# Performance work log

Measured on AMD Instinct MI355X. Metric: run time of the kernel, lower is better.

## Reference

```python
import jax, jax.numpy as jnp
import numpy as np

B, K, T, C = 4, 8, 2048, 64

def setup_inputs() -> dict:
    key = jax.random.key(0)
    ks = jax.random.split(key, 7)
    return {
        "x": jax.random.normal(ks[0], (B, K, T, C), dtype=jnp.float32),
        "Wq": jax.random.normal(ks[1], (C, C), dtype=jnp.float32) / np.sqrt(C),
        "bq": jax.random.normal(ks[2], (C,), dtype=jnp.float32) * 0.01,
        "Wk": jax.random.normal(ks[3], (C, C), dtype=jnp.float32) / np.sqrt(C),
        "bk": jax.random.normal(ks[4], (C,), dtype=jnp.float32) * 0.01,
        "Wv": jax.random.normal(ks[5], (C, C), dtype=jnp.float32) / np.sqrt(C),
        "bv": jax.random.normal(ks[6], (C,), dtype=jnp.float32) * 0.01,
    }

def reference(x, Wq, bq, Wk, bk, Wv, bv):
    c_dim = x.shape[-1]
    # torch nn.Linear: y = x @ W.T + b
    q = jnp.einsum('bktc,dc->bktd', x, Wq) + bq
    k = jnp.einsum('bktc,dc->bktd', x, Wk) + bk
    v = jnp.einsum('bktc,dc->bktd', x, Wv) + bv
    scores = jnp.einsum('bkic,bkjc->bkij', q, k) / jnp.sqrt(jnp.float32(c_dim))
    attn = jax.nn.softmax(scores, axis=-1)
    out = jnp.einsum('bkij,bkjc->bkic', attn, v)
    return out
```

## Files before the change

### kernel.cpp

```cpp
#include <hip/hip_runtime.h>


#define T_DIM 2048
#define NHEAD 32
#define NKT   (T_DIM / 64)
#define QSCALE 0.18033688011112042f
#define SOFF  8.0f

#define SWZ(row, grp) ((row) * 64 + ((((grp) ^ ((row) & 7)) & 7) * 8) + (((grp) & 8) * 8))

typedef _Float16 h8 __attribute__((ext_vector_type(8)));
typedef _Float16 h4 __attribute__((ext_vector_type(4)));
typedef __fp16   g2 __attribute__((ext_vector_type(2)));
typedef float    f4 __attribute__((ext_vector_type(4)));

union H4U { h4 v; g2 p[2]; };

__device__ inline h4 cvt4(f4 x) {
    H4U u;
    u.p[0] = __builtin_amdgcn_cvt_pkrtz(x[0], x[1]);
    u.p[1] = __builtin_amdgcn_cvt_pkrtz(x[2], x[3]);
    return u.v;
}

__global__ __launch_bounds__(256) void qkv_proj_kernel(
    const float* __restrict__ x,
    const float* __restrict__ Wq, const float* __restrict__ bq,
    const float* __restrict__ Wk, const float* __restrict__ bk,
    const float* __restrict__ Wv, const float* __restrict__ bv,
    _Float16* __restrict__ qh, _Float16* __restrict__ kh,
    _Float16* __restrict__ vt)
{
    __shared__ _Float16 xs[128 * 64];
    __shared__ _Float16 ws[3][64 * 64];
    __shared__ _Float16 ot[128 * 64];
    __shared__ float bsh[3][64];

    const int tid  = threadIdx.x;
    const int row0 = blockIdx.x * 128;
    const int head = blockIdx.x >> 4;
    const int t0   = (blockIdx.x & 15) * 128;

    {
        const float* xb = x + (size_t)row0 * 64;
        #pragma unroll
        for (int pass = 0; pass < 8; ++pass) {
            const int idx = pass * 1024 + tid * 4;
            const int r = idx >> 6, c = idx & 63;
            f4 xv = *(const f4*)(xb + idx);
            *(h4*)&xs[SWZ(r, c >> 3) + (c & 7)] = cvt4(xv);
        }
    }
    #pragma unroll
    for (int m = 0; m < 3; ++m) {
        const float* Wm = (m == 0) ? Wq : ((m == 1) ? Wk : Wv);
        const float* bm = (m == 0) ? bq : ((m == 1) ? bk : bv);
        #pragma unroll
        for (int pass = 0; pass < 4; ++pass) {
            const int idx = pass * 1024 + tid * 4;
            const int d = idx >> 6, c = idx & 63;
            f4 wv = *(const f4*)(Wm + idx);
            *(h4*)&ws[m][SWZ(d, c >> 3) + (c & 7)] = cvt4(wv);
        }
        if (tid < 64) bsh[m][tid] = bm[tid];
    }
    __syncthreads();

    const int w    = tid >> 6;
    const int lane = tid & 63;
    const int l15  = lane & 15;
    const int qd   = lane >> 4;

    h8 af[2][2];
    #pragma unroll
    for (int mt = 0; mt < 2; ++mt)
        #pragma unroll
        for (int ch = 0; ch < 2; ++ch) {
            const int r = w * 32 + mt * 16 + l15;
            af[mt][ch] = *(const h8*)&xs[SWZ(r, ch * 4 + qd)];
        }

    #pragma unroll
    for (int m = 0; m < 3; ++m) {
        h8 bf[4][2];
        #pragma unroll
        for (int ns = 0; ns < 4; ++ns)
            #pragma unroll
            for (int ch = 0; ch < 2; ++ch)
                bf[ns][ch] = *(const h8*)&ws[m][SWZ(ns * 16 + l15, ch * 4 + qd)];

        f4 acc[2][4];
        #pragma unroll
        for (int mt = 0; mt < 2; ++mt)
            #pragma unroll
            for (int ns = 0; ns < 4; ++ns)
                acc[mt][ns] = (f4){0.f, 0.f, 0.f, 0.f};
        #pragma unroll
        for (int ch = 0; ch < 2; ++ch)
            #pragma unroll
            for (int mt = 0; mt < 2; ++mt)
                #pragma unroll
                for (int ns = 0; ns < 4; ++ns)
                    acc[mt][ns] = __builtin_amdgcn_mfma_f32_16x16x32_f16(
                        af[mt][ch], bf[ns][ch], acc[mt][ns], 0, 0, 0);

        __syncthreads();
        if (m < 2) {
            #pragma unroll
            for (int mt = 0; mt < 2; ++mt)
                #pragma unroll
                for (int ns = 0; ns < 4; ++ns) {
                    const int d = ns * 16 + l15;
                    const float bias = bsh[m][d];
                    #pragma unroll
                    for (int r = 0; r < 4; ++r) {
                        const int t = w * 32 + mt * 16 + qd * 4 + r;
                        float v = acc[mt][ns][r] + bias;
                        if (m == 0) v *= QSCALE;
                        ot[SWZ(t, d >> 3) + (d & 7)] = (_Float16)v;
                    }
                }
            __syncthreads();
            _Float16* dst = (m == 0) ? qh : kh;
            #pragma unroll
            for (int pass = 0; pass < 4; ++pass) {
                const int t  = pass * 32 + (tid >> 3);
                const int c0 = (tid & 7) * 8;
                *(h8*)&dst[(size_t)(row0 + t) * 64 + c0] =
                    *(const h8*)&ot[SWZ(t, tid & 7)];
            }
        } else {
            #pragma unroll
            for (int mt = 0; mt < 2; ++mt)
                #pragma unroll
                for (int ns = 0; ns < 4; ++ns) {
                    const int d = ns * 16 + l15;
                    const float bias = bsh[2][d];
                    const int tl = w * 32 + mt * 16 + qd * 4;
                    h4 pv;
                    #pragma unroll
                    for (int r = 0; r < 4; ++r)
                        pv[r] = (_Float16)(acc[mt][ns][r] + bias);
                    const int g = tl >> 3;
                    *(h4*)&ot[d * 128 + ((g ^ (d & 7)) & 7) * 8 + ((g & 8) * 8) + (tl & 7)] = pv;
                }
            __syncthreads();
            #pragma unroll
            for (int pass = 0; pass < 4; ++pass) {
                const int idx = pass * 2048 + tid * 8;
                const int d = idx >> 7, tl = idx & 127;
                const int g = tl >> 3;
                h8 val = *(const h8*)&ot[d * 128 + ((g ^ (d & 7)) & 7) * 8 + ((g & 8) * 8)];
                *(h8*)&vt[(size_t)(head * 64 + d) * T_DIM + t0 + tl] = val;
            }
        }
    }
}

__global__ __launch_bounds__(256) void attn_kernel(
    const _Float16* __restrict__ qh, const _Float16* __restrict__ kh,
    const _Float16* __restrict__ vt, float* __restrict__ out)
{
    __shared__ _Float16 kts[64 * 64];
    __shared__ _Float16 vts[64 * 64];
    const int tid  = threadIdx.x;
    const int w    = tid >> 6;
    const int lane = tid & 63;
    const int l15  = lane & 15;
    const int qd   = lane >> 4;
    const int head = blockIdx.x >> 4;
    const int qt   = blockIdx.x & 15;
    const int q0   = qt * 128 + w * 32;

    h8 qf[2][2];
    #pragma unroll
    for (int is = 0; is < 2; ++is) {
        const _Float16* qp = qh + (size_t)(head * T_DIM + q0 + is * 16 + l15) * 64 + qd * 8;
        qf[is][0] = *(const h8*)qp;
        qf[is][1] = *(const h8*)(qp + 32);
    }

    float l_s[2] = {0.f, 0.f};
    f4 oacc[2][4];
    #pragma unroll
    for (int is = 0; is < 2; ++is)
        #pragma unroll
        for (int cs = 0; cs < 4; ++cs)
            oacc[is][cs] = (f4){0.f, 0.f, 0.f, 0.f};

    const size_t kbase = (size_t)head * T_DIM * 64;
    const int srow = tid >> 3;
    const int sgrp = tid & 7;
    const _Float16* kg = kh + kbase + (size_t)srow * 64 + sgrp * 8;
    const _Float16* vg = vt + kbase + (size_t)srow * T_DIM + sgrp * 8;
    _Float16* kl0 = &kts[SWZ(srow, sgrp)];
    _Float16* kl1 = &kts[SWZ(srow + 32, sgrp)];
    _Float16* vl0 = &vts[SWZ(srow, sgrp)];
    _Float16* vl1 = &vts[SWZ(srow + 32, sgrp)];

    h8 kr0 = *(const h8*)(kg);
    h8 kr1 = *(const h8*)(kg + (size_t)32 * 64);
    h8 vr0 = *(const h8*)(vg);
    h8 vr1 = *(const h8*)(vg + (size_t)32 * T_DIM);

    for (int kt = 0; kt < NKT; ++kt) {
        __syncthreads();
        *(h8*)kl0 = kr0; *(h8*)kl1 = kr1;
        *(h8*)vl0 = vr0; *(h8*)vl1 = vr1;
        __syncthreads();
        if (kt + 1 < NKT) {
            const _Float16* kg1 = kg + (size_t)(kt + 1) * 4096;
            const _Float16* vg1 = vg + (size_t)(kt + 1) * 64;
            kr0 = *(const h8*)(kg1);
            kr1 = *(const h8*)(kg1 + (size_t)32 * 64);
            vr0 = *(const h8*)(vg1);
            vr1 = *(const h8*)(vg1 + (size_t)32 * T_DIM);
        }

        f4 st[4][2];
        #pragma unroll
        for (int jt = 0; jt < 4; ++jt)
            #pragma unroll
            for (int is = 0; is < 2; ++is)
                st[jt][is] = (f4){-SOFF, -SOFF, -SOFF, -SOFF};
        #pragma unroll
        for (int ch = 0; ch < 2; ++ch)
            #pragma unroll
            for (int jt = 0; jt < 4; ++jt) {
                h8 kf = *(const h8*)&kts[SWZ(jt * 16 + l15, ch * 4 + qd)];
                #pragma unroll
                for (int is = 0; is < 2; ++is)
                    st[jt][is] = __builtin_amdgcn_mfma_f32_16x16x32_f16(
                        kf, qf[is][ch], st[jt][is], 0, 0, 0);
            }

        h4 pf[4][2];
        #pragma unroll
        for (int is = 0; is < 2; ++is) {
            float rs = 0.f;
            #pragma unroll
            for (int jt = 0; jt < 4; ++jt) {
                float p0 = __builtin_exp2f(st[jt][is][0]);
                float p1 = __builtin_exp2f(st[jt][is][1]);
                float p2 = __builtin_exp2f(st[jt][is][2]);
                float p3 = __builtin_exp2f(st[jt][is][3]);
                rs += (p0 + p1) + (p2 + p3);
                H4U u;
                u.p[0] = __builtin_amdgcn_cvt_pkrtz(p0, p1);
                u.p[1] = __builtin_amdgcn_cvt_pkrtz(p2, p3);
                pf[jt][is] = u.v;
            }
            l_s[is] += rs;
        }

        #pragma unroll
        for (int jt = 0; jt < 4; ++jt)
            #pragma unroll
            for (int cs = 0; cs < 4; ++cs) {
                h4 vf = *(const h4*)&vts[SWZ(cs * 16 + l15, jt * 2 + (qd >> 1)) + (qd & 1) * 4];
                #pragma unroll
                for (int is = 0; is < 2; ++is)
                    oacc[is][cs] = __builtin_amdgcn_mfma_f32_16x16x16f16(
                        pf[jt][is], vf, oacc[is][cs], 0, 0, 0);
            }
    }

    #pragma unroll
    for (int is = 0; is < 2; ++is) {
        float l = l_s[is];
        l += __shfl_xor(l, 16, 64);
        l += __shfl_xor(l, 32, 64);
        float linv[4];
        #pragma unroll
        for (int r = 0; r < 4; ++r)
            linv[r] = 1.f / __shfl(l, qd * 4 + r, 64);
        #pragma unroll
        for (int cs = 0; cs < 4; ++cs) {
            const int c = cs * 16 + l15;
            #pragma unroll
            for (int r = 0; r < 4; ++r) {
                const int t = q0 + is * 16 + qd * 4 + r;
                out[(size_t)(head * T_DIM + t) * 64 + c] = oacc[is][cs][r] * linv[r];
            }
        }
    }
}

extern "C" void kernel_launch(void* const* d_in, const int* in_sizes, int n_in,
                              void* d_out, int out_size, void* d_ws, size_t ws_size,
                              hipStream_t stream)
{
    (void)in_sizes; (void)n_in; (void)out_size; (void)ws_size;
    const float* x  = (const float*)d_in[0];
    const float* Wq = (const float*)d_in[1];
    const float* bq = (const float*)d_in[2];
    const float* Wk = (const float*)d_in[3];
    const float* bk = (const float*)d_in[4];
    const float* Wv = (const float*)d_in[5];
    const float* bv = (const float*)d_in[6];
    float* out = (float*)d_out;

    _Float16* qh = (_Float16*)d_ws;
    _Float16* kh = qh + (size_t)NHEAD * T_DIM * 64;
    _Float16* vt = kh + (size_t)NHEAD * T_DIM * 64;

    hipLaunchKernelGGL(qkv_proj_kernel, dim3(512), dim3(256), 0, stream,
                       x, Wq, bq, Wk, bk, Wv, bv, qh, kh, vt);
    hipLaunchKernelGGL(attn_kernel, dim3(NHEAD * 16), dim3(256), 0, stream,
                       qh, kh, vt, out);
}
```

Baseline: 149.2 us.

## Double-buffer K/V tiles in attention and shrink blocks for more parallelism

The attention kernel now keeps two LDS buffers for the K and V tiles. The next tile is written into the spare buffer after the current tile's MFMAs, which cuts the loop to one barrier per iteration. Blocks drop to 128 threads and the grid doubles to 1024, with block IDs remapped so that heads are grouped per XCD for better L2 locality. The QKV projection also moves to 64-row blocks and loads x straight into registers, removing the LDS staging buffer. The trade-offs are more K/V register staging and re-loading K/V once per smaller query tile.

```diff
diff --git a/kernel.cpp b/kernel.cpp
--- a/kernel.cpp
+++ b/kernel.cpp
@@ -7,7 +7,7 @@
 #define QSCALE 0.18033688011112042f
 #define SOFF  8.0f
 
-#define SWZ(row, grp) ((row) * 64 + ((((grp) ^ ((row) & 7)) & 7) * 8) + (((grp) & 8) * 8))
+#define SWZ(row, grp) ((row) * 64 + ((((grp) ^ ((row) & 7)) & 7) * 8))
 
 typedef _Float16 h8 __attribute__((ext_vector_type(8)));
 typedef _Float16 h4 __attribute__((ext_vector_type(4)));
@@ -21,6 +21,18 @@
     u.p[0] = __builtin_amdgcn_cvt_pkrtz(x[0], x[1]);
     u.p[1] = __builtin_amdgcn_cvt_pkrtz(x[2], x[3]);
     return u.v;
+}
+
+__device__ inline h8 cvt8(f4 a, f4 b) {
+    h8 r;
+    H4U u;
+    u.p[0] = __builtin_amdgcn_cvt_pkrtz(a[0], a[1]);
+    u.p[1] = __builtin_amdgcn_cvt_pkrtz(a[2], a[3]);
+    r[0] = u.v[0]; r[1] = u.v[1]; r[2] = u.v[2]; r[3] = u.v[3];
+    u.p[0] = __builtin_amdgcn_cvt_pkrtz(b[0], b[1]);
+    u.p[1] = __builtin_amdgcn_cvt_pkrtz(b[2], b[3]);
+    r[4] = u.v[0]; r[5] = u.v[1]; r[6] = u.v[2]; r[7] = u.v[3];
+    return r;
 }
 
 __global__ __launch_bounds__(256) void qkv_proj_kernel(
@@ -31,26 +43,15 @@
     _Float16* __restrict__ qh, _Float16* __restrict__ kh,
     _Float16* __restrict__ vt)
 {
-    __shared__ _Float16 xs[128 * 64];
     __shared__ _Float16 ws[3][64 * 64];
-    __shared__ _Float16 ot[128 * 64];
+    __shared__ _Float16 ot[64 * 64];
     __shared__ float bsh[3][64];
 
     const int tid  = threadIdx.x;
-    const int row0 = blockIdx.x * 128;
-    const int head = blockIdx.x >> 4;
-    const int t0   = (blockIdx.x & 15) * 128;
-
-    {
-        const float* xb = x + (size_t)row0 * 64;
-        #pragma unroll
-        for (int pass = 0; pass < 8; ++pass) {
-            const int idx = pass * 1024 + tid * 4;
-            const int r = idx >> 6, c = idx & 63;
-            f4 xv = *(const f4*)(xb + idx);
-            *(h4*)&xs[SWZ(r, c >> 3) + (c & 7)] = cvt4(xv);
-        }
-    }
+    const int row0 = blockIdx.x * 64;
+    const int head = blockIdx.x >> 5;
+    const int t0   = (blockIdx.x & 31) * 64;
+
     #pragma unroll
     for (int m = 0; m < 3; ++m) {
         const float* Wm = (m == 0) ? Wq : ((m == 1) ? Wk : Wv);
@@ -64,21 +65,23 @@
         }
         if (tid < 64) bsh[m][tid] = bm[tid];
     }
-    __syncthreads();
 
     const int w    = tid >> 6;
     const int lane = tid & 63;
     const int l15  = lane & 15;
     const int qd   = lane >> 4;
 
-    h8 af[2][2];
-    #pragma unroll
-    for (int mt = 0; mt < 2; ++mt)
+    h8 af[2];
+    {
+        const float* xp = x + (size_t)(row0 + w * 16 + l15) * 64 + qd * 8;
         #pragma unroll
         for (int ch = 0; ch < 2; ++ch) {
-            const int r = w * 32 + mt * 16 + l15;
-            af[mt][ch] = *(const h8*)&xs[SWZ(r, ch * 4 + qd)];
-        }
+            f4 a0 = *(const f4*)(xp + ch * 32);
+            f4 a1 = *(const f4*)(xp + ch * 32 + 4);
+            af[ch] = cvt8(a0, a1);
+        }
+    }
+    __syncthreads();
 
     #pragma unroll
     for (int m = 0; m < 3; ++m) {
@@ -89,41 +92,35 @@
             for (int ch = 0; ch < 2; ++ch)
                 bf[ns][ch] = *(const h8*)&ws[m][SWZ(ns * 16 + l15, ch * 4 + qd)];
 
-        f4 acc[2][4];
-        #pragma unroll
-        for (int mt = 0; mt < 2; ++mt)
+        f4 acc[4];
+        #pragma unroll
+        for (int ns = 0; ns < 4; ++ns)
+            acc[ns] = (f4){0.f, 0.f, 0.f, 0.f};
+        #pragma unroll
+        for (int ch = 0; ch < 2; ++ch)
             #pragma unroll
             for (int ns = 0; ns < 4; ++ns)
-                acc[mt][ns] = (f4){0.f, 0.f, 0.f, 0.f};
-        #pragma unroll
-        for (int ch = 0; ch < 2; ++ch)
-            #pragma unroll
-            for (int mt = 0; mt < 2; ++mt)
-                #pragma unroll
-                for (int ns = 0; ns < 4; ++ns)
-                    acc[mt][ns] = __builtin_amdgcn_mfma_f32_16x16x32_f16(
-                        af[mt][ch], bf[ns][ch], acc[mt][ns], 0, 0, 0);
+                acc[ns] = __builtin_amdgcn_mfma_f32_16x16x32_f16(
+                    af[ch], bf[ns][ch], acc[ns], 0, 0, 0);
 
         __syncthreads();
         if (m < 2) {
             #pragma unroll
-            for (int mt = 0; mt < 2; ++mt)
+            for (int ns = 0; ns < 4; ++ns) {
+                const int d = ns * 16 + l15;
+                const float bias = bsh[m][d];
                 #pragma unroll
-                for (int ns = 0; ns < 4; ++ns) {
-                    const int d = ns * 16 + l15;
-                    const float bias = bsh[m][d];
-                    #pragma unroll
-                    for (int r = 0; r < 4; ++r) {
-                        const int t = w * 32 + mt * 16 + qd * 4 + r;
-                        float v = acc[mt][ns][r] + bias;
-                        if (m == 0) v *= QSCALE;
-                        ot[SWZ(t, d >> 3) + (d & 7)] = (_Float16)v;
-                    }
+                for (int r = 0; r < 4; ++r) {
+                    const int t = w * 16 + qd * 4 + r;
+                    float v = acc[ns][r] + bias;
+                    if (m == 0) v *= QSCALE;
+                    ot[SWZ(t, d >> 3) + (d & 7)] = (_Float16)v;
                 }
+            }
             __syncthreads();
             _Float16* dst = (m == 0) ? qh : kh;
             #pragma unroll
-            for (int pass = 0; pass < 4; ++pass) {
+            for (int pass = 0; pass < 2; ++pass) {
                 const int t  = pass * 32 + (tid >> 3);
                 const int c0 = (tid & 7) * 8;
                 *(h8*)&dst[(size_t)(row0 + t) * 64 + c0] =
@@ -131,46 +128,46 @@
             }
         } else {
             #pragma unroll
-            for (int mt = 0; mt < 2; ++mt)
+            for (int ns = 0; ns < 4; ++ns) {
+                const int d = ns * 16 + l15;
+                const float bias = bsh[2][d];
+                const int tl = w * 16 + qd * 4;
+                h4 pv;
                 #pragma unroll
-                for (int ns = 0; ns < 4; ++ns) {
-                    const int d = ns * 16 + l15;
-                    const float bias = bsh[2][d];
-                    const int tl = w * 32 + mt * 16 + qd * 4;
-                    h4 pv;
-                    #pragma unroll
-                    for (int r = 0; r < 4; ++r)
-                        pv[r] = (_Float16)(acc[mt][ns][r] + bias);
-                    const int g = tl >> 3;
-                    *(h4*)&ot[d * 128 + ((g ^ (d & 7)) & 7) * 8 + ((g & 8) * 8) + (tl & 7)] = pv;
-                }
+                for (int r = 0; r < 4; ++r)
+                    pv[r] = (_Float16)(acc[ns][r] + bias);
+                *(h4*)&ot[SWZ(d, tl >> 3) + (tl & 7)] = pv;
+            }
             __syncthreads();
             #pragma unroll
-            for (int pass = 0; pass < 4; ++pass) {
+            for (int pass = 0; pass < 2; ++pass) {
                 const int idx = pass * 2048 + tid * 8;
-                const int d = idx >> 7, tl = idx & 127;
-                const int g = tl >> 3;
-                h8 val = *(const h8*)&ot[d * 128 + ((g ^ (d & 7)) & 7) * 8 + ((g & 8) * 8)];
+                const int d = idx >> 6, tl = idx & 63;
+                h8 val = *(const h8*)&ot[SWZ(d, tl >> 3)];
                 *(h8*)&vt[(size_t)(head * 64 + d) * T_DIM + t0 + tl] = val;
             }
         }
     }
 }
 
-__global__ __launch_bounds__(256) void attn_kernel(
+__global__ __launch_bounds__(128) void attn_kernel(
     const _Float16* __restrict__ qh, const _Float16* __restrict__ kh,
     const _Float16* __restrict__ vt, float* __restrict__ out)
 {
-    __shared__ _Float16 kts[64 * 64];
-    __shared__ _Float16 vts[64 * 64];
+    __shared__ _Float16 kts[2][64 * 64];
+    __shared__ _Float16 vts[2][64 * 64];
     const int tid  = threadIdx.x;
     const int w    = tid >> 6;
     const int lane = tid & 63;
     const int l15  = lane & 15;
     const int qd   = lane >> 4;
-    const int head = blockIdx.x >> 4;
-    const int qt   = blockIdx.x & 15;
-    const int q0   = qt * 128 + w * 32;
+
+    const int bid   = blockIdx.x;
+    const int xcd   = bid & 7;
+    const int slot  = bid >> 3;
+    const int head  = xcd * 4 + (slot >> 5);
+    const int qpart = slot & 31;
+    const int q0    = qpart * 64 + w * 32;
 
     h8 qf[2][2];
     #pragma unroll
@@ -193,28 +190,30 @@
     const int sgrp = tid & 7;
     const _Float16* kg = kh + kbase + (size_t)srow * 64 + sgrp * 8;
     const _Float16* vg = vt + kbase + (size_t)srow * T_DIM + sgrp * 8;
-    _Float16* kl0 = &kts[SWZ(srow, sgrp)];
-    _Float16* kl1 = &kts[SWZ(srow + 32, sgrp)];
-    _Float16* vl0 = &vts[SWZ(srow, sgrp)];
-    _Float16* vl1 = &vts[SWZ(srow + 32, sgrp)];
-
-    h8 kr0 = *(const h8*)(kg);
-    h8 kr1 = *(const h8*)(kg + (size_t)32 * 64);
-    h8 vr0 = *(const h8*)(vg);
-    h8 vr1 = *(const h8*)(vg + (size_t)32 * T_DIM);
+
+    h8 kr[4], vr[4];
+    #pragma unroll
+    for (int ii = 0; ii < 4; ++ii) {
+        kr[ii] = *(const h8*)(kg + ii * 1024);
+        vr[ii] = *(const h8*)(vg + ii * 32768);
+    }
+    #pragma unroll
+    for (int ii = 0; ii < 4; ++ii) {
+        *(h8*)&kts[0][SWZ(srow + ii * 16, sgrp)] = kr[ii];
+        *(h8*)&vts[0][SWZ(srow + ii * 16, sgrp)] = vr[ii];
+    }
+    __syncthreads();
 
     for (int kt = 0; kt < NKT; ++kt) {
-        __syncthreads();
-        *(h8*)kl0 = kr0; *(h8*)kl1 = kr1;
-        *(h8*)vl0 = vr0; *(h8*)vl1 = vr1;
-        __syncthreads();
+        const int buf = kt & 1;
         if (kt + 1 < NKT) {
             const _Float16* kg1 = kg + (size_t)(kt + 1) * 4096;
             const _Float16* vg1 = vg + (size_t)(kt + 1) * 64;
-            kr0 = *(const h8*)(kg1);
-            kr1 = *(const h8*)(kg1 + (size_t)32 * 64);
-            vr0 = *(const h8*)(vg1);
-            vr1 = *(const h8*)(vg1 + (size_t)32 * T_DIM);
+            #pragma unroll
+            for (int ii = 0; ii < 4; ++ii) {
+                kr[ii] = *(const h8*)(kg1 + ii * 1024);
+                vr[ii] = *(const h8*)(vg1 + ii * 32768);
+            }
         }
 
         f4 st[4][2];
@@ -227,7 +226,7 @@
         for (int ch = 0; ch < 2; ++ch)
             #pragma unroll
             for (int jt = 0; jt < 4; ++jt) {
-                h8 kf = *(const h8*)&kts[SWZ(jt * 16 + l15, ch * 4 + qd)];
+                h8 kf = *(const h8*)&kts[buf][SWZ(jt * 16 + l15, ch * 4 + qd)];
                 #pragma unroll
                 for (int is = 0; is < 2; ++is)
                     st[jt][is] = __builtin_amdgcn_mfma_f32_16x16x32_f16(
@@ -257,12 +256,21 @@
         for (int jt = 0; jt < 4; ++jt)
             #pragma unroll
             for (int cs = 0; cs < 4; ++cs) {
-                h4 vf = *(const h4*)&vts[SWZ(cs * 16 + l15, jt * 2 + (qd >> 1)) + (qd & 1) * 4];
+                h4 vf = *(const h4*)&vts[buf][SWZ(cs * 16 + l15, jt * 2 + (qd >> 1)) + (qd & 1) * 4];
                 #pragma unroll
                 for (int is = 0; is < 2; ++is)
                     oacc[is][cs] = __builtin_amdgcn_mfma_f32_16x16x16f16(
                         pf[jt][is], vf, oacc[is][cs], 0, 0, 0);
             }
+
+        if (kt + 1 < NKT) {
+            #pragma unroll
+            for (int ii = 0; ii < 4; ++ii) {
+                *(h8*)&kts[1 - buf][SWZ(srow + ii * 16, sgrp)] = kr[ii];
+                *(h8*)&vts[1 - buf][SWZ(srow + ii * 16, sgrp)] = vr[ii];
+            }
+        }
+        __syncthreads();
     }
 
     #pragma unroll
@@ -304,8 +312,8 @@
     _Float16* kh = qh + (size_t)NHEAD * T_DIM * 64;
     _Float16* vt = kh + (size_t)NHEAD * T_DIM * 64;
 
-    hipLaunchKernelGGL(qkv_proj_kernel, dim3(512), dim3(256), 0, stream,
+    hipLaunchKernelGGL(qkv_proj_kernel, dim3(1024), dim3(256), 0, stream,
                        x, Wq, bq, Wk, bk, Wv, bv, qh, kh, vt);
-    hipLaunchKernelGGL(attn_kernel, dim3(NHEAD * 16), dim3(256), 0, stream,
+    hipLaunchKernelGGL(attn_kernel, dim3(1024), dim3(128), 0, stream,
                        qh, kh, vt, out);
 }
```

Result: slower. 160.1 us (+7.3%).
